# Performance work log

Measured on AMD Instinct MI355X. Metric: run time of the kernel, lower is better.

Reference implementation:

```python
import jax, jax.numpy as jnp
import numpy as np


def _reduce1(x):
    # x: [B, n, d] -> [B, 2d]; exists=max, forall=min over objects (exclude_self is a no-op for cnt=1)
    return jnp.concatenate([x.max(axis=1), x.min(axis=1)], axis=-1)


def _reduce2(x):
    # x: [B, n, n, d] -> [B, n, 2d]; exclude_self masks diagonal i==j (0 for exists/max, 1 for forall/min)
    n = x.shape[1]
    diag = jnp.eye(n, dtype=bool)[None, :, :, None]
    exists = jnp.where(diag, 0.0, x).max(axis=2)
    forall = jnp.where(diag, 1.0, x).min(axis=2)
    return jnp.concatenate([exists, forall], axis=-1)


def _layer(f0, f1, f2, p):
    # One LogicLayer step (breadth=2, minmax reducer, exclude_self, sigmoid norm, no hidden layers)
    W0, b0, W1, b1, W2, b2 = p
    B, n, d1 = f1.shape
    # order 0: [self, reduce(order1)]
    g0 = jnp.concatenate([f0, _reduce1(f1)], axis=-1)
    o0 = jax.nn.sigmoid(g0 @ W0 + b0)
    # order 1: [expand(order0), self, reduce(order2)]
    e0 = jnp.broadcast_to(f0[:, None, :], (B, n, f0.shape[-1]))
    g1 = jnp.concatenate([e0, f1, _reduce2(f2)], axis=-1)
    o1 = jax.nn.sigmoid(g1 @ W1 + b1)
    # order 2: [expand(order1), self] then Permutation(2) = cat(x, swap(i,j))
    e1 = jnp.broadcast_to(f1[:, :, None, :], (B, n, n, d1))
    g2 = jnp.concatenate([e1, f2], axis=-1)
    g2 = jnp.concatenate([g2, jnp.swapaxes(g2, 1, 2)], axis=-1)
    o2 = jax.nn.sigmoid(g2 @ W2 + b2)
    return o0, o1, o2


def setup_inputs() -> dict:
    key = jax.random.key(0)
    B, n = 4, 256
    d = [32, 64, 64]
    O = 128
    ks = iter(jax.random.split(key, 64))
    inp = {
        "x0": jax.random.uniform(next(ks), (B, d[0]), dtype=jnp.float32),
        "x1": jax.random.uniform(next(ks), (B, n, d[1]), dtype=jnp.float32),
        "x2": jax.random.uniform(next(ks), (B, n, n, d[2]), dtype=jnp.float32),
    }
    fan_ins = [
        (d[0] + 2 * d[1], d[0] + d[1] + 2 * d[2], 2 * (d[1] + d[2])),  # layer 0
        (O + 2 * O, O + O + 2 * O, 2 * (O + O)),                        # layer 1
        (O + 2 * O, O + O + 2 * O, 2 * (O + O)),                        # layer 2
    ]
    for l, fins in enumerate(fan_ins):
        for o, fin in enumerate(fins):
            inp[f"W{o}_{l}"] = jax.random.normal(next(ks), (fin, O), dtype=jnp.float32) / np.sqrt(fin).astype(np.float32)
            inp[f"b{o}_{l}"] = jnp.zeros((O,), dtype=jnp.float32)
    return inp


def reference(x0, x1, x2,
              W0_0, b0_0, W1_0, b1_0, W2_0, b2_0,
              W0_1, b0_1, W1_1, b1_1, W2_1, b2_1,
              W0_2, b0_2, W1_2, b1_2, W2_2, b2_2):
    f = (x0, x1, x2)
    for p in ((W0_0, b0_0, W1_0, b1_0, W2_0, b2_0),
              (W0_1, b0_1, W1_1, b1_1, W2_1, b2_1),
              (W0_2, b0_2, W1_2, b1_2, W2_2, b2_2)):
        f = _layer(*f, p)
    return f
```

## Files before the change

### kernel.cpp

```cpp
#include <hip/hip_runtime.h>
#include <hip/hip_bf16.h>
#include <cstdint>

#define NN 256
#define NB 4
#define OC 128

using bf16x8_t = __attribute__((ext_vector_type(8))) __bf16;
using f32x4_t  = __attribute__((ext_vector_type(4))) float;

typedef const __attribute__((address_space(1))) uint8_t* gptr1_t;
typedef __attribute__((address_space(3))) uint8_t* lptr3_t;

__device__ __forceinline__ void async_load16(const void* g, void* l) {
  __builtin_amdgcn_global_load_lds((gptr1_t)g, (lptr3_t)l, 16, 0, 0);
}

__device__ __forceinline__ float sigf(float x) {
  return 1.0f / (1.0f + __expf(-x));
}

__device__ __forceinline__ uint16_t f2bf_rne(float f) {
  uint32_t u = __float_as_uint(f);
  uint32_t r = (u + 0x7fffu + ((u >> 16) & 1u)) >> 16;
  return (uint16_t)r;
}

__global__ __launch_bounds__(256) void reduce2_l0_kernel(
    const float* __restrict__ x2, float* __restrict__ r2,
    uint16_t* __restrict__ x2bf) {
  const int bid = blockIdx.x;
  const int b = bid >> 8, i = bid & 255;
  const int tid = threadIdx.x;
  const int q = tid & 15, s = tid >> 4;
  const size_t rowbase = ((size_t)(b * NN + i) * NN) * 64 + q * 4;
  float mx0 = 0.f, mx1 = 0.f, mx2 = 0.f, mx3 = 0.f;
  float mn0 = 1.f, mn1 = 1.f, mn2 = 1.f, mn3 = 1.f;
  for (int j = s; j < NN; j += 16) {
    const float4 x = *(const float4*)(x2 + rowbase + (size_t)j * 64);
    uint2 pk;
    pk.x = (uint32_t)f2bf_rne(x.x) | ((uint32_t)f2bf_rne(x.y) << 16);
    pk.y = (uint32_t)f2bf_rne(x.z) | ((uint32_t)f2bf_rne(x.w) << 16);
    *(uint2*)(x2bf + rowbase + (size_t)j * 64) = pk;
    if (j != i) {
      mx0 = fmaxf(mx0, x.x); mx1 = fmaxf(mx1, x.y);
      mx2 = fmaxf(mx2, x.z); mx3 = fmaxf(mx3, x.w);
      mn0 = fminf(mn0, x.x); mn1 = fminf(mn1, x.y);
      mn2 = fminf(mn2, x.z); mn3 = fminf(mn3, x.w);
    }
  }
  __shared__ float4 smx[256], smn[256];
  smx[tid] = make_float4(mx0, mx1, mx2, mx3);
  smn[tid] = make_float4(mn0, mn1, mn2, mn3);
  __syncthreads();
  if (s == 0) {
    for (int ss = 1; ss < 16; ++ss) {
      float4 a = smx[q + ss * 16], c = smn[q + ss * 16];
      mx0 = fmaxf(mx0, a.x); mx1 = fmaxf(mx1, a.y);
      mx2 = fmaxf(mx2, a.z); mx3 = fmaxf(mx3, a.w);
      mn0 = fminf(mn0, c.x); mn1 = fminf(mn1, c.y);
      mn2 = fminf(mn2, c.z); mn3 = fminf(mn3, c.w);
    }
    float* r = r2 + (size_t)(b * NN + i) * 128;
    r[q * 4 + 0] = mx0; r[q * 4 + 1] = mx1; r[q * 4 + 2] = mx2; r[q * 4 + 3] = mx3;
    r[64 + q * 4 + 0] = mn0; r[64 + q * 4 + 1] = mn1;
    r[64 + q * 4 + 2] = mn2; r[64 + q * 4 + 3] = mn3;
  }
}

__device__ __forceinline__ void emit_wt(const float* __restrict__ W2,
                                        uint16_t* __restrict__ Wt, int d1,
                                        int d2, int idx) {
  const int K = 2 * d2;
  const int nn = idx / K, k = idx - nn * K;
  const int row = (k < d2) ? (d1 + k) : (2 * d1 + d2 + (k - d2));
  Wt[idx] = f2bf_rne(W2[row * OC + nn]);
}

__global__ void prep_wt_all(const float* __restrict__ W20,
                            const float* __restrict__ W21,
                            const float* __restrict__ W22,
                            uint16_t* __restrict__ Wt0,
                            uint16_t* __restrict__ Wt1,
                            uint16_t* __restrict__ Wt2) {
  const int g = blockIdx.x * 256 + threadIdx.x;
  if (g < 16384) emit_wt(W20, Wt0, 64, 64, g);
  else if (g < 16384 + 32768) emit_wt(W21, Wt1, 128, 128, g - 16384);
  else emit_wt(W22, Wt2, 128, 128, g - 49152);
}

template <int D0, int D1, int D2, bool HAS_NEXT>
__global__ __launch_bounds__(256) void small_kernel(
    const float* __restrict__ f0in, const float* __restrict__ f1in,
    const float* __restrict__ r2in, const float* __restrict__ W0,
    const float* __restrict__ b0, const float* __restrict__ W1,
    const float* __restrict__ b1, const float* __restrict__ W2,
    const float* __restrict__ b2, float* __restrict__ f0out,
    float* __restrict__ f1out, float* __restrict__ u, float* __restrict__ v,
    float* __restrict__ r2n) {
  constexpr int FIN1 = D0 + D1 + 2 * D2;
  constexpr int FIN0 = D0 + 2 * D1;
  constexpr int ROWS = 4;
  const int blk = blockIdx.x;
  const int bi0 = blk * ROWS;
  const int b = bi0 >> 8;
  const int tid = threadIdx.x;
  const int c = tid & 127, s = tid >> 7;

  __shared__ float g1[ROWS][FIN1];
  __shared__ float part[3][ROWS][2][128];
  __shared__ float g0[FIN0];
  __shared__ float rmx[256], rmn[256];

  for (int r = 0; r < ROWS; ++r) {
    const int bi = bi0 + r;
    for (int k = tid; k < FIN1; k += 256) {
      float x;
      if (k < D0) x = f0in[b * D0 + k];
      else if (k < D0 + D1) x = f1in[(size_t)bi * D1 + (k - D0)];
      else x = r2in[(size_t)bi * (2 * D2) + (k - D0 - D1)];
      g1[r][k] = x;
    }
  }
  __syncthreads();

  float a1[ROWS] = {0.f, 0.f, 0.f, 0.f};
  constexpr int H1 = FIN1 / 2;
#pragma unroll 4
  for (int k = s * H1; k < s * H1 + H1; ++k) {
    const float w = W1[(size_t)k * OC + c];
#pragma unroll
    for (int r = 0; r < ROWS; ++r) a1[r] += g1[r][k] * w;
  }
  float au[ROWS] = {0.f, 0.f, 0.f, 0.f};
  float av[ROWS] = {0.f, 0.f, 0.f, 0.f};
  constexpr int H2 = D1 / 2;
#pragma unroll 4
  for (int k = s * H2; k < s * H2 + H2; ++k) {
    const float wu = W2[(size_t)k * OC + c];
    const float wv = W2[(size_t)(D1 + D2 + k) * OC + c];
#pragma unroll
    for (int r = 0; r < ROWS; ++r) {
      const float x = g1[r][D0 + k];
      au[r] += x * wu;
      av[r] += x * wv;
    }
  }
#pragma unroll
  for (int r = 0; r < ROWS; ++r) {
    part[0][r][s][c] = a1[r];
    part[1][r][s][c] = au[r];
    part[2][r][s][c] = av[r];
  }
  __syncthreads();
  if (s == 0) {
#pragma unroll
    for (int r = 0; r < ROWS; ++r) {
      const size_t bi = bi0 + r;
      f1out[bi * OC + c] = sigf(a1[r] + part[0][r][1][c] + b1[c]);
      u[bi * OC + c] = au[r] + part[1][r][1][c] + b2[c];
      v[bi * OC + c] = av[r] + part[2][r][1][c];
    }
  }
  if (HAS_NEXT) {
#pragma unroll
    for (int r = 0; r < ROWS; ++r)
      r2n[(size_t)(bi0 + r) * 256 + s * 128 + c] = (s == 0) ? 0.f : 1.f;
  }

  if ((blk & 63) == 0) {
    constexpr int S = 256 / D1;
    const int cc = tid & (D1 - 1), ss = tid / D1;
    float mx = -1e30f, mn = 1e30f;
    for (int j = ss; j < NN; j += S) {
      const float x = f1in[((size_t)b * NN + j) * D1 + cc];
      mx = fmaxf(mx, x); mn = fminf(mn, x);
    }
    rmx[tid] = mx; rmn[tid] = mn;
    __syncthreads();
    if (ss == 0) {
      for (int s2 = 1; s2 < S; ++s2) {
        mx = fmaxf(mx, rmx[cc + s2 * D1]);
        mn = fminf(mn, rmn[cc + s2 * D1]);
      }
      g0[D0 + cc] = mx;
      g0[D0 + D1 + cc] = mn;
    }
    if (tid < D0) g0[tid] = f0in[b * D0 + tid];
    __syncthreads();
    if (tid < OC) {
      float acc = b0[tid];
#pragma unroll 8
      for (int k = 0; k < FIN0; ++k) acc += g0[k] * W0[k * OC + tid];
      f0out[b * OC + tid] = sigf(acc);
    }
  }
}

template <int D2, typename OUT_T, bool REDUCE>
__global__ __launch_bounds__(256, 3) void gemm2_kernel(
    const __hip_bfloat16* __restrict__ f2, const uint16_t* __restrict__ Wt,
    const float* __restrict__ u, const float* __restrict__ v,
    OUT_T* __restrict__ out, float* __restrict__ r2n) {
  constexpr int K = 2 * D2;
  constexpr int NCH = K / 64;
  constexpr bool BF16OUT = (sizeof(OUT_T) == 2);
  constexpr int LDSB = BF16OUT ? (128 * 272) : 32768;
  const int bid = blockIdx.x;
  const int jt = bid & 1, i = (bid >> 1) & 255, b = bid >> 9;
  const int j0 = jt * 128;
  const int tid = threadIdx.x;
  const int wv = tid >> 6, lane = tid & 63;
  const int wr = wv >> 1, wc = wv & 1;
  const int l15 = lane & 15, l4 = lane >> 4;

  __shared__ __align__(16) uint8_t lds[LDSB];
  __shared__ unsigned smax[128], smin[128];
  uint8_t* const ldsA = lds;
  uint8_t* const ldsW = lds + 16384;

  const __hip_bfloat16* A1 = f2 + ((size_t)(b * NN + i) * NN + j0) * D2;
  const __hip_bfloat16* A2 = f2 + ((size_t)(b * NN + j0) * NN + i) * D2;

  f32x4_t acc[4][4];
#pragma unroll
  for (int a = 0; a < 4; ++a)
#pragma unroll
    for (int q = 0; q < 4; ++q) acc[a][q] = (f32x4_t){0.f, 0.f, 0.f, 0.f};

  for (int c = 0; c < NCH; ++c) {
    const int kbg = c * 64;
    const bool second = (kbg >= D2);
    const __hip_bfloat16* Ab = second ? A2 : A1;
    const size_t rstride = second ? (size_t)NN * D2 : (size_t)D2;
    const int kbase = second ? (kbg - D2) : kbg;
#pragma unroll
    for (int q = 0; q < 4; ++q) {
      const int id = wv * 4 + q;
      const int mi = id & 7, ks = id >> 3;
      const int row = mi * 16 + l15;
      const int kk = ks * 32 + l4 * 8;
      async_load16(Ab + (size_t)row * rstride + kbase + kk, ldsA + id * 1024);
    }
#pragma unroll
    for (int q = 0; q < 4; ++q) {
      const int id = wv * 4 + q;
      const int ni = id & 7, ks = id >> 3;
      const int nn2 = ni * 16 + l15;
      const int kk = ks * 32 + l4 * 8;
      async_load16(Wt + (size_t)nn2 * K + kbg + kk, ldsW + id * 1024);
    }
    __syncthreads();
#pragma unroll
    for (int ks = 0; ks < 2; ++ks) {
      bf16x8_t Af[4], Bf[4];
#pragma unroll
      for (int a = 0; a < 4; ++a)
        Af[a] = *(const bf16x8_t*)(ldsA + ((ks * 8 + wr * 4 + a) << 10) + (lane << 4));
#pragma unroll
      for (int q = 0; q < 4; ++q)
        Bf[q] = *(const bf16x8_t*)(ldsW + ((ks * 8 + wc * 4 + q) << 10) + (lane << 4));
#pragma unroll
      for (int a = 0; a < 4; ++a)
#pragma unroll
        for (int q = 0; q < 4; ++q)
          acc[a][q] = __builtin_amdgcn_mfma_f32_16x16x32_bf16(Af[a], Bf[q],
                                                              acc[a][q], 0, 0, 0);
    }
    __syncthreads();
  }

  const size_t bi2 = (size_t)(b * NN + i);
  float uval[4];
#pragma unroll
  for (int q = 0; q < 4; ++q) uval[q] = u[bi2 * OC + wc * 64 + q * 16 + l15];
  const size_t obase = (bi2 * NN + j0) * OC;
  const size_t vbase = (size_t)(b * NN + j0) * OC;

  if (BF16OUT) {
    if (REDUCE && tid < 128) { smax[tid] = 0u; smin[tid] = 0x3f800000u; }
    __syncthreads();
    float lmx[4] = {0.f, 0.f, 0.f, 0.f};
    float lmn[4] = {1.f, 1.f, 1.f, 1.f};
#pragma unroll
    for (int a = 0; a < 4; ++a) {
      const int rowb = wr * 64 + a * 16 + l4 * 4;
#pragma unroll
      for (int r = 0; r < 4; ++r) {
        const int j = rowb + r;
        const bool excl = (j0 + j) == i;
#pragma unroll
        for (int q = 0; q < 4; ++q) {
          const int col = wc * 64 + q * 16 + l15;
          const float x = acc[a][q][r] + uval[q] + v[vbase + (size_t)j * OC + col];
          const float sg = sigf(x);
          *(uint16_t*)(lds + j * 272 + col * 2) = f2bf_rne(sg);
          if (REDUCE && !excl) {
            lmx[q] = fmaxf(lmx[q], sg);
            lmn[q] = fminf(lmn[q], sg);
          }
        }
      }
    }
    if (REDUCE) {
#pragma unroll
      for (int q = 0; q < 4; ++q) {
        const int col = wc * 64 + q * 16 + l15;
        atomicMax(&smax[col], __float_as_uint(lmx[q]));
        atomicMin(&smin[col], __float_as_uint(lmn[q]));
      }
    }
    __syncthreads();
    uint16_t* const outp = (uint16_t*)out;
#pragma unroll
    for (int ci = 0; ci < 8; ++ci) {
      const int chunk = ci * 256 + tid;
      const int row = chunk >> 4, off = chunk & 15;
      const uint4 val = *(const uint4*)(lds + row * 272 + off * 16);
      *(uint4*)(outp + obase + (size_t)row * OC + off * 8) = val;
    }
    if (REDUCE && tid < 128) {
      unsigned* const r2u = (unsigned*)r2n;
      atomicMax(&r2u[bi2 * 256 + tid], smax[tid]);
      atomicMin(&r2u[bi2 * 256 + 128 + tid], smin[tid]);
    }
  } else {
    float* const outp = (float*)out;
#pragma unroll
    for (int a = 0; a < 4; ++a) {
      const int rowb = wr * 64 + a * 16 + l4 * 4;
#pragma unroll
      for (int r = 0; r < 4; ++r) {
        const int j = rowb + r;
#pragma unroll
        for (int q = 0; q < 4; ++q) {
          const int col = wc * 64 + q * 16 + l15;
          const float x = acc[a][q][r] + uval[q] + v[vbase + (size_t)j * OC + col];
          outp[obase + (size_t)j * OC + col] = sigf(x);
        }
      }
    }
  }
}

extern "C" void kernel_launch(void* const* d_in, const int* in_sizes, int n_in,
                              void* d_out, int out_size, void* d_ws,
                              size_t ws_size, hipStream_t stream) {
  const float* x0 = (const float*)d_in[0];
  const float* x1 = (const float*)d_in[1];
  const float* x2 = (const float*)d_in[2];
  const float *Wp[3][3], *bp[3][3];
  for (int l = 0; l < 3; ++l)
    for (int o = 0; o < 3; ++o) {
      Wp[l][o] = (const float*)d_in[3 + l * 6 + o * 2];
      bp[l][o] = (const float*)d_in[3 + l * 6 + o * 2 + 1];
    }

  const size_t F2E = (size_t)NB * NN * NN * OC;
  const size_t X2E = (size_t)NB * NN * NN * 64;

  uint8_t* ws = (uint8_t*)d_ws;
  size_t off = 0;
  auto carve = [&](size_t bytes) -> uint8_t* {
    uint8_t* p = ws + off;
    off += (bytes + 255) & ~(size_t)255;
    return p;
  };
  float* f0a = (float*)carve((size_t)NB * OC * 4);
  float* f0b = (float*)carve((size_t)NB * OC * 4);
  float* f1a = (float*)carve((size_t)NB * NN * OC * 4);
  float* f1b = (float*)carve((size_t)NB * NN * OC * 4);
  float* r2a = (float*)carve((size_t)NB * NN * 128 * 4);
  float* r2b = (float*)carve((size_t)NB * NN * 256 * 4);
  float* r2c = (float*)carve((size_t)NB * NN * 256 * 4);
  float* uu  = (float*)carve((size_t)NB * NN * OC * 4);
  float* vv  = (float*)carve((size_t)NB * NN * OC * 4);
  uint16_t* Wt0 = (uint16_t*)carve((size_t)OC * 128 * 2);
  uint16_t* Wt1 = (uint16_t*)carve((size_t)OC * 256 * 2);
  uint16_t* Wt2 = (uint16_t*)carve((size_t)OC * 256 * 2);
  __hip_bfloat16* f2a = (__hip_bfloat16*)carve(F2E * 2);

  __hip_bfloat16* f2b;
  uint16_t* x2bf;
  if (ws_size >= off + F2E * 2) {
    f2b = (__hip_bfloat16*)carve(F2E * 2);
    x2bf = (uint16_t*)f2b;
  } else {
    f2b = (__hip_bfloat16*)d_in[2];
    x2bf = (uint16_t*)carve(X2E * 2);
  }

  float* out_f0 = (float*)d_out;
  float* out_f1 = out_f0 + (size_t)NB * OC;
  float* out_f2 = out_f1 + (size_t)NB * NN * OC;

  prep_wt_all<<<320, 256, 0, stream>>>(Wp[0][2], Wp[1][2], Wp[2][2], Wt0, Wt1,
                                       Wt2);
  reduce2_l0_kernel<<<NB * NN, 256, 0, stream>>>(x2, r2a, x2bf);

  small_kernel<32, 64, 64, true><<<NB * NN / 4, 256, 0, stream>>>(
      x0, x1, r2a, Wp[0][0], bp[0][0], Wp[0][1], bp[0][1], Wp[0][2], bp[0][2],
      f0a, f1a, uu, vv, r2b);
  gemm2_kernel<64, __hip_bfloat16, true><<<NB * NN * 2, 256, 0, stream>>>(
      (const __hip_bfloat16*)x2bf, Wt0, uu, vv, f2a, r2b);

  small_kernel<128, 128, 128, true><<<NB * NN / 4, 256, 0, stream>>>(
      f0a, f1a, r2b, Wp[1][0], bp[1][0], Wp[1][1], bp[1][1], Wp[1][2], bp[1][2],
      f0b, f1b, uu, vv, r2c);
  gemm2_kernel<128, __hip_bfloat16, true><<<NB * NN * 2, 256, 0, stream>>>(
      f2a, Wt1, uu, vv, f2b, r2c);

  small_kernel<128, 128, 128, false><<<NB * NN / 4, 256, 0, stream>>>(
      f0b, f1b, r2c, Wp[2][0], bp[2][0], Wp[2][1], bp[2][1], Wp[2][2], bp[2][2],
      out_f0, out_f1, uu, vv, nullptr);
  gemm2_kernel<128, float, false><<<NB * NN * 2, 256, 0, stream>>>(
      f2b, Wt2, uu, vv, out_f2, nullptr);
}
```

Before: 584.8 us.

## Replace scalar order-0/1 small kernel with bf16 MFMA GEMM on packed inputs

Replaces the per-layer scalar FP32 small_kernel, which computed the order-1 linear layer and the u/v projections, with a bf16 MFMA GEMM. Its operands are a packed bf16 activation matrix and a bf16 weight matrix built once at startup from W1 and W2. Order-0 work moves to a separate tiny kernel that also broadcasts f0 into the next layer's packed input. A small conversion kernel packs the reduced r2 into the same buffer. The aim is to cut the FP32 FMA cost of the small matmuls, at the price of bf16 rounding on order-1 inputs, several extra launches, and only 48 blocks in the GEMM.

```diff
diff --git a/kernel.cpp b/kernel.cpp
--- a/kernel.cpp
+++ b/kernel.cpp
@@ -26,14 +26,62 @@
   return (uint16_t)r;
 }
 
+__device__ __forceinline__ void emit_wt(const float* __restrict__ W2,
+                                        uint16_t* __restrict__ Wt, int d1,
+                                        int d2, int idx) {
+  const int K = 2 * d2;
+  const int nn = idx / K, k = idx - nn * K;
+  const int row = (k < d2) ? (d1 + k) : (2 * d1 + d2 + (k - d2));
+  Wt[idx] = f2bf_rne(W2[row * OC + nn]);
+}
+
+__device__ __forceinline__ void emit_bt(const float* __restrict__ W1,
+                                        const float* __restrict__ W2,
+                                        uint16_t* __restrict__ Bt, int D0,
+                                        int D1, int D2, int FIN1, int KP,
+                                        int idx) {
+  const int n = idx / KP, k = idx - n * KP;
+  float val = 0.f;
+  if (n < 128) {
+    if (k < FIN1) val = W1[k * OC + n];
+  } else if (n < 256) {
+    if (k >= D0 && k < D0 + D1) val = W2[(k - D0) * OC + (n - 128)];
+  } else {
+    if (k >= D0 && k < D0 + D1) val = W2[(D1 + D2 + (k - D0)) * OC + (n - 256)];
+  }
+  Bt[idx] = f2bf_rne(val);
+}
+
+__global__ __launch_bounds__(256) void prep_all(
+    const float* __restrict__ W2_0, const float* __restrict__ W2_1,
+    const float* __restrict__ W2_2, const float* __restrict__ W1_0,
+    const float* __restrict__ W1_1, const float* __restrict__ W1_2,
+    uint16_t* __restrict__ Wt0, uint16_t* __restrict__ Wt1,
+    uint16_t* __restrict__ Wt2, uint16_t* __restrict__ Bt0,
+    uint16_t* __restrict__ Bt1, uint16_t* __restrict__ Bt2) {
+  int g = blockIdx.x * 256 + threadIdx.x;
+  if (g < 16384) { emit_wt(W2_0, Wt0, 64, 64, g); return; }
+  g -= 16384;
+  if (g < 32768) { emit_wt(W2_1, Wt1, 128, 128, g); return; }
+  g -= 32768;
+  if (g < 32768) { emit_wt(W2_2, Wt2, 128, 128, g); return; }
+  g -= 32768;
+  if (g < 98304) { emit_bt(W1_0, W2_0, Bt0, 32, 64, 64, 224, 256, g); return; }
+  g -= 98304;
+  if (g < 196608) { emit_bt(W1_1, W2_1, Bt1, 128, 128, 128, 512, 512, g); return; }
+  g -= 196608;
+  if (g < 196608) { emit_bt(W1_2, W2_2, Bt2, 128, 128, 128, 512, 512, g); }
+}
+
 __global__ __launch_bounds__(256) void reduce2_l0_kernel(
-    const float* __restrict__ x2, float* __restrict__ r2,
-    uint16_t* __restrict__ x2bf) {
+    const float* __restrict__ x2, const float* __restrict__ x0,
+    const float* __restrict__ x1, uint16_t* __restrict__ g1bf0,
+    uint16_t* __restrict__ x2bf, float* __restrict__ r2init) {
   const int bid = blockIdx.x;
   const int b = bid >> 8, i = bid & 255;
   const int tid = threadIdx.x;
   const int q = tid & 15, s = tid >> 4;
-  const size_t rowbase = ((size_t)(b * NN + i) * NN) * 64 + q * 4;
+  const size_t rowbase = ((size_t)bid * NN) * 64 + q * 4;
   float mx0 = 0.f, mx1 = 0.f, mx2 = 0.f, mx3 = 0.f;
   float mn0 = 1.f, mn1 = 1.f, mn2 = 1.f, mn3 = 1.f;
   for (int j = s; j < NN; j += 16) {
@@ -53,6 +101,7 @@
   smx[tid] = make_float4(mx0, mx1, mx2, mx3);
   smn[tid] = make_float4(mn0, mn1, mn2, mn3);
   __syncthreads();
+  uint16_t* const g = g1bf0 + (size_t)bid * 256;
   if (s == 0) {
     for (int ss = 1; ss < 16; ++ss) {
       float4 a = smx[q + ss * 16], c = smn[q + ss * 16];
@@ -61,140 +110,161 @@
       mn0 = fminf(mn0, c.x); mn1 = fminf(mn1, c.y);
       mn2 = fminf(mn2, c.z); mn3 = fminf(mn3, c.w);
     }
-    float* r = r2 + (size_t)(b * NN + i) * 128;
-    r[q * 4 + 0] = mx0; r[q * 4 + 1] = mx1; r[q * 4 + 2] = mx2; r[q * 4 + 3] = mx3;
-    r[64 + q * 4 + 0] = mn0; r[64 + q * 4 + 1] = mn1;
-    r[64 + q * 4 + 2] = mn2; r[64 + q * 4 + 3] = mn3;
-  }
-}
-
-__device__ __forceinline__ void emit_wt(const float* __restrict__ W2,
-                                        uint16_t* __restrict__ Wt, int d1,
-                                        int d2, int idx) {
-  const int K = 2 * d2;
-  const int nn = idx / K, k = idx - nn * K;
-  const int row = (k < d2) ? (d1 + k) : (2 * d1 + d2 + (k - d2));
-  Wt[idx] = f2bf_rne(W2[row * OC + nn]);
-}
-
-__global__ void prep_wt_all(const float* __restrict__ W20,
-                            const float* __restrict__ W21,
-                            const float* __restrict__ W22,
-                            uint16_t* __restrict__ Wt0,
-                            uint16_t* __restrict__ Wt1,
-                            uint16_t* __restrict__ Wt2) {
-  const int g = blockIdx.x * 256 + threadIdx.x;
-  if (g < 16384) emit_wt(W20, Wt0, 64, 64, g);
-  else if (g < 16384 + 32768) emit_wt(W21, Wt1, 128, 128, g - 16384);
-  else emit_wt(W22, Wt2, 128, 128, g - 49152);
-}
-
-template <int D0, int D1, int D2, bool HAS_NEXT>
-__global__ __launch_bounds__(256) void small_kernel(
-    const float* __restrict__ f0in, const float* __restrict__ f1in,
-    const float* __restrict__ r2in, const float* __restrict__ W0,
-    const float* __restrict__ b0, const float* __restrict__ W1,
-    const float* __restrict__ b1, const float* __restrict__ W2,
-    const float* __restrict__ b2, float* __restrict__ f0out,
-    float* __restrict__ f1out, float* __restrict__ u, float* __restrict__ v,
-    float* __restrict__ r2n) {
-  constexpr int FIN1 = D0 + D1 + 2 * D2;
-  constexpr int FIN0 = D0 + 2 * D1;
-  constexpr int ROWS = 4;
-  const int blk = blockIdx.x;
-  const int bi0 = blk * ROWS;
-  const int b = bi0 >> 8;
+    g[96 + q * 4 + 0] = f2bf_rne(mx0); g[96 + q * 4 + 1] = f2bf_rne(mx1);
+    g[96 + q * 4 + 2] = f2bf_rne(mx2); g[96 + q * 4 + 3] = f2bf_rne(mx3);
+    g[160 + q * 4 + 0] = f2bf_rne(mn0); g[160 + q * 4 + 1] = f2bf_rne(mn1);
+    g[160 + q * 4 + 2] = f2bf_rne(mn2); g[160 + q * 4 + 3] = f2bf_rne(mn3);
+  }
+  if (tid < 32) g[tid] = f2bf_rne(x0[b * 32 + tid]);
+  else if (tid < 96) g[tid] = f2bf_rne(x1[(size_t)bid * 64 + tid - 32]);
+  else if (tid >= 224) g[tid] = 0;
+  r2init[(size_t)bid * 256 + tid] = (tid < 128) ? 0.f : 1.f;
+}
+
+template <int D0, int D1, bool DUP>
+__global__ __launch_bounds__(256) void o0_kernel(
+    const float* __restrict__ f0, const float* __restrict__ f1,
+    const float* __restrict__ W0, const float* __restrict__ b0,
+    float* __restrict__ f0out, uint16_t* __restrict__ g1next) {
+  constexpr int FIN = D0 + 2 * D1;
+  constexpr int S = 256 / D1;
+  const int b = blockIdx.x;
   const int tid = threadIdx.x;
-  const int c = tid & 127, s = tid >> 7;
-
-  __shared__ float g1[ROWS][FIN1];
-  __shared__ float part[3][ROWS][2][128];
-  __shared__ float g0[FIN0];
-  __shared__ float rmx[256], rmn[256];
-
-  for (int r = 0; r < ROWS; ++r) {
-    const int bi = bi0 + r;
-    for (int k = tid; k < FIN1; k += 256) {
-      float x;
-      if (k < D0) x = f0in[b * D0 + k];
-      else if (k < D0 + D1) x = f1in[(size_t)bi * D1 + (k - D0)];
-      else x = r2in[(size_t)bi * (2 * D2) + (k - D0 - D1)];
-      g1[r][k] = x;
-    }
-  }
-  __syncthreads();
-
-  float a1[ROWS] = {0.f, 0.f, 0.f, 0.f};
-  constexpr int H1 = FIN1 / 2;
-#pragma unroll 4
-  for (int k = s * H1; k < s * H1 + H1; ++k) {
-    const float w = W1[(size_t)k * OC + c];
-#pragma unroll
-    for (int r = 0; r < ROWS; ++r) a1[r] += g1[r][k] * w;
-  }
-  float au[ROWS] = {0.f, 0.f, 0.f, 0.f};
-  float av[ROWS] = {0.f, 0.f, 0.f, 0.f};
-  constexpr int H2 = D1 / 2;
-#pragma unroll 4
-  for (int k = s * H2; k < s * H2 + H2; ++k) {
-    const float wu = W2[(size_t)k * OC + c];
-    const float wv = W2[(size_t)(D1 + D2 + k) * OC + c];
-#pragma unroll
-    for (int r = 0; r < ROWS; ++r) {
-      const float x = g1[r][D0 + k];
-      au[r] += x * wu;
-      av[r] += x * wv;
-    }
-  }
-#pragma unroll
-  for (int r = 0; r < ROWS; ++r) {
-    part[0][r][s][c] = a1[r];
-    part[1][r][s][c] = au[r];
-    part[2][r][s][c] = av[r];
-  }
+  const int c = tid & (D1 - 1), s = tid / D1;
+  __shared__ float g0[FIN];
+  __shared__ float smx[256], smn[256];
+  __shared__ float sval[128];
+  float mx = -1e30f, mn = 1e30f;
+  const float* f1b = f1 + (size_t)b * NN * D1;
+  for (int j = s; j < NN; j += S) {
+    float x = f1b[(size_t)j * D1 + c];
+    mx = fmaxf(mx, x); mn = fminf(mn, x);
+  }
+  smx[tid] = mx; smn[tid] = mn;
   __syncthreads();
   if (s == 0) {
-#pragma unroll
-    for (int r = 0; r < ROWS; ++r) {
-      const size_t bi = bi0 + r;
-      f1out[bi * OC + c] = sigf(a1[r] + part[0][r][1][c] + b1[c]);
-      u[bi * OC + c] = au[r] + part[1][r][1][c] + b2[c];
-      v[bi * OC + c] = av[r] + part[2][r][1][c];
-    }
-  }
-  if (HAS_NEXT) {
-#pragma unroll
-    for (int r = 0; r < ROWS; ++r)
-      r2n[(size_t)(bi0 + r) * 256 + s * 128 + c] = (s == 0) ? 0.f : 1.f;
-  }
-
-  if ((blk & 63) == 0) {
-    constexpr int S = 256 / D1;
-    const int cc = tid & (D1 - 1), ss = tid / D1;
-    float mx = -1e30f, mn = 1e30f;
-    for (int j = ss; j < NN; j += S) {
-      const float x = f1in[((size_t)b * NN + j) * D1 + cc];
-      mx = fmaxf(mx, x); mn = fminf(mn, x);
-    }
-    rmx[tid] = mx; rmn[tid] = mn;
-    __syncthreads();
-    if (ss == 0) {
-      for (int s2 = 1; s2 < S; ++s2) {
-        mx = fmaxf(mx, rmx[cc + s2 * D1]);
-        mn = fminf(mn, rmn[cc + s2 * D1]);
+    for (int ss = 1; ss < S; ++ss) {
+      mx = fmaxf(mx, smx[c + ss * D1]);
+      mn = fminf(mn, smn[c + ss * D1]);
+    }
+    g0[D0 + c] = mx;
+    g0[D0 + D1 + c] = mn;
+  }
+  if (tid < D0) g0[tid] = f0[b * D0 + tid];
+  __syncthreads();
+  if (tid < OC) {
+    float acc = b0[tid];
+#pragma unroll 8
+    for (int k = 0; k < FIN; ++k) acc += g0[k] * W0[k * OC + tid];
+    const float val = sigf(acc);
+    f0out[b * OC + tid] = val;
+    sval[tid] = val;
+  }
+  if (DUP) {
+    __syncthreads();
+    for (int idx = tid; idx < 256 * 128; idx += 256) {
+      const int row = idx >> 7, cc = idx & 127;
+      g1next[((size_t)(b * 256 + row)) * 512 + cc] = f2bf_rne(sval[cc]);
+    }
+  }
+}
+
+template <int KP, bool DUP>
+__global__ __launch_bounds__(256) void small_gemm(
+    const uint16_t* __restrict__ g1, const uint16_t* __restrict__ Bt,
+    const float* __restrict__ b1, const float* __restrict__ b2,
+    float* __restrict__ f1out, uint16_t* __restrict__ g1next,
+    float* __restrict__ u, float* __restrict__ v) {
+  constexpr int NCH = KP / 64;
+  const int bid = blockIdx.x;
+  const int mt = bid / 3, nt = bid - mt * 3;
+  const int m0 = mt * 64, n0 = nt * 128;
+  const int tid = threadIdx.x;
+  const int wv = tid >> 6, lane = tid & 63;
+  const int l15 = lane & 15, l4 = lane >> 4;
+
+  __shared__ __align__(16) uint8_t ldsA[8192];
+  __shared__ __align__(16) uint8_t ldsB[16384];
+
+  f32x4_t acc[4][2];
+#pragma unroll
+  for (int a = 0; a < 4; ++a)
+#pragma unroll
+    for (int q = 0; q < 2; ++q) acc[a][q] = (f32x4_t){0.f, 0.f, 0.f, 0.f};
+
+  for (int c = 0; c < NCH; ++c) {
+    const int kbg = c * 64;
+#pragma unroll
+    for (int t = 0; t < 2; ++t) {
+      const int id = wv * 2 + t;
+      const int mi = id & 3, ks = id >> 2;
+      async_load16(g1 + (size_t)(m0 + mi * 16 + l15) * KP + kbg + ks * 32 + l4 * 8,
+                   ldsA + id * 1024);
+    }
+#pragma unroll
+    for (int t = 0; t < 4; ++t) {
+      const int id = wv * 4 + t;
+      const int ni = id & 7, ks = id >> 3;
+      async_load16(Bt + (size_t)(n0 + ni * 16 + l15) * KP + kbg + ks * 32 + l4 * 8,
+                   ldsB + id * 1024);
+    }
+    __syncthreads();
+#pragma unroll
+    for (int ks = 0; ks < 2; ++ks) {
+      bf16x8_t Af[4], Bf[2];
+#pragma unroll
+      for (int a = 0; a < 4; ++a)
+        Af[a] = *(const bf16x8_t*)(ldsA + ((ks * 4 + a) << 10) + (lane << 4));
+#pragma unroll
+      for (int q = 0; q < 2; ++q)
+        Bf[q] = *(const bf16x8_t*)(ldsB + ((ks * 8 + wv * 2 + q) << 10) + (lane << 4));
+#pragma unroll
+      for (int a = 0; a < 4; ++a)
+#pragma unroll
+        for (int q = 0; q < 2; ++q)
+          acc[a][q] = __builtin_amdgcn_mfma_f32_16x16x32_bf16(Af[a], Bf[q],
+                                                              acc[a][q], 0, 0, 0);
+    }
+    __syncthreads();
+  }
+
+  float bias[2];
+#pragma unroll
+  for (int q = 0; q < 2; ++q) {
+    const int cc = wv * 32 + q * 16 + l15;
+    bias[q] = (nt == 0) ? b1[cc] : ((nt == 1) ? b2[cc] : 0.f);
+  }
+#pragma unroll
+  for (int a = 0; a < 4; ++a) {
+    const int rl = a * 16 + l4 * 4;
+#pragma unroll
+    for (int r = 0; r < 4; ++r) {
+      const size_t bi = m0 + rl + r;
+#pragma unroll
+      for (int q = 0; q < 2; ++q) {
+        const int cc = wv * 32 + q * 16 + l15;
+        const float x = acc[a][q][r] + bias[q];
+        if (nt == 0) {
+          const float val = sigf(x);
+          f1out[bi * OC + cc] = val;
+          if (DUP) g1next[bi * 512 + 128 + cc] = f2bf_rne(val);
+        } else if (nt == 1) {
+          u[bi * OC + cc] = x;
+        } else {
+          v[bi * OC + cc] = x;
+        }
       }
-      g0[D0 + cc] = mx;
-      g0[D0 + D1 + cc] = mn;
-    }
-    if (tid < D0) g0[tid] = f0in[b * D0 + tid];
-    __syncthreads();
-    if (tid < OC) {
-      float acc = b0[tid];
-#pragma unroll 8
-      for (int k = 0; k < FIN0; ++k) acc += g0[k] * W0[k * OC + tid];
-      f0out[b * OC + tid] = sigf(acc);
-    }
-  }
+    }
+  }
+}
+
+template <bool INIT_NEXT>
+__global__ __launch_bounds__(256) void conv_r2_kernel(
+    const float* __restrict__ r2, uint16_t* __restrict__ g1next,
+    float* __restrict__ r2next) {
+  const int bi = blockIdx.x, t = threadIdx.x;
+  g1next[(size_t)bi * 512 + 256 + t] = f2bf_rne(r2[(size_t)bi * 256 + t]);
+  if (INIT_NEXT) r2next[(size_t)bi * 256 + t] = (t < 128) ? 0.f : 1.f;
 }
 
 template <int D2, typename OUT_T, bool REDUCE>
@@ -370,7 +440,6 @@
   float* f0b = (float*)carve((size_t)NB * OC * 4);
   float* f1a = (float*)carve((size_t)NB * NN * OC * 4);
   float* f1b = (float*)carve((size_t)NB * NN * OC * 4);
-  float* r2a = (float*)carve((size_t)NB * NN * 128 * 4);
   float* r2b = (float*)carve((size_t)NB * NN * 256 * 4);
   float* r2c = (float*)carve((size_t)NB * NN * 256 * 4);
   float* uu  = (float*)carve((size_t)NB * NN * OC * 4);
@@ -378,6 +447,12 @@
   uint16_t* Wt0 = (uint16_t*)carve((size_t)OC * 128 * 2);
   uint16_t* Wt1 = (uint16_t*)carve((size_t)OC * 256 * 2);
   uint16_t* Wt2 = (uint16_t*)carve((size_t)OC * 256 * 2);
+  uint16_t* Bt0 = (uint16_t*)carve((size_t)384 * 256 * 2);
+  uint16_t* Bt1 = (uint16_t*)carve((size_t)384 * 512 * 2);
+  uint16_t* Bt2 = (uint16_t*)carve((size_t)384 * 512 * 2);
+  uint16_t* g1bf0 = (uint16_t*)carve((size_t)NB * NN * 256 * 2);
+  uint16_t* g1bf1 = (uint16_t*)carve((size_t)NB * NN * 512 * 2);
+  uint16_t* g1bf2 = (uint16_t*)carve((size_t)NB * NN * 512 * 2);
   __hip_bfloat16* f2a = (__hip_bfloat16*)carve(F2E * 2);
 
   __hip_bfloat16* f2b;
@@ -394,25 +469,31 @@
   float* out_f1 = out_f0 + (size_t)NB * OC;
   float* out_f2 = out_f1 + (size_t)NB * NN * OC;
 
-  prep_wt_all<<<320, 256, 0, stream>>>(Wp[0][2], Wp[1][2], Wp[2][2], Wt0, Wt1,
-                                       Wt2);
-  reduce2_l0_kernel<<<NB * NN, 256, 0, stream>>>(x2, r2a, x2bf);
-
-  small_kernel<32, 64, 64, true><<<NB * NN / 4, 256, 0, stream>>>(
-      x0, x1, r2a, Wp[0][0], bp[0][0], Wp[0][1], bp[0][1], Wp[0][2], bp[0][2],
-      f0a, f1a, uu, vv, r2b);
+  prep_all<<<2240, 256, 0, stream>>>(Wp[0][2], Wp[1][2], Wp[2][2], Wp[0][1],
+                                     Wp[1][1], Wp[2][1], Wt0, Wt1, Wt2, Bt0,
+                                     Bt1, Bt2);
+  reduce2_l0_kernel<<<NB * NN, 256, 0, stream>>>(x2, x0, x1, g1bf0, x2bf, r2b);
+
+  o0_kernel<32, 64, true><<<NB, 256, 0, stream>>>(x0, x1, Wp[0][0], bp[0][0],
+                                                  f0a, g1bf1);
+  small_gemm<256, true><<<48, 256, 0, stream>>>(g1bf0, Bt0, bp[0][1], bp[0][2],
+                                                f1a, g1bf1, uu, vv);
   gemm2_kernel<64, __hip_bfloat16, true><<<NB * NN * 2, 256, 0, stream>>>(
       (const __hip_bfloat16*)x2bf, Wt0, uu, vv, f2a, r2b);
-
-  small_kernel<128, 128, 128, true><<<NB * NN / 4, 256, 0, stream>>>(
-      f0a, f1a, r2b, Wp[1][0], bp[1][0], Wp[1][1], bp[1][1], Wp[1][2], bp[1][2],
-      f0b, f1b, uu, vv, r2c);
+  conv_r2_kernel<true><<<NB * NN, 256, 0, stream>>>(r2b, g1bf1, r2c);
+
+  o0_kernel<128, 128, true><<<NB, 256, 0, stream>>>(f0a, f1a, Wp[1][0],
+                                                    bp[1][0], f0b, g1bf2);
+  small_gemm<512, true><<<48, 256, 0, stream>>>(g1bf1, Bt1, bp[1][1], bp[1][2],
+                                                f1b, g1bf2, uu, vv);
   gemm2_kernel<128, __hip_bfloat16, true><<<NB * NN * 2, 256, 0, stream>>>(
       f2a, Wt1, uu, vv, f2b, r2c);
-
-  small_kernel<128, 128, 128, false><<<NB * NN / 4, 256, 0, stream>>>(
-      f0b, f1b, r2c, Wp[2][0], bp[2][0], Wp[2][1], bp[2][1], Wp[2][2], bp[2][2],
-      out_f0, out_f1, uu, vv, nullptr);
+  conv_r2_kernel<false><<<NB * NN, 256, 0, stream>>>(r2c, g1bf2, nullptr);
+
+  o0_kernel<128, 128, false><<<NB, 256, 0, stream>>>(f0b, f1b, Wp[2][0],
+                                                     bp[2][0], out_f0, nullptr);
+  small_gemm<512, false><<<48, 256, 0, stream>>>(g1bf2, Bt2, bp[2][1], bp[2][2],
+                                                 out_f1, nullptr, uu, vv);
   gemm2_kernel<128, float, false><<<NB * NN * 2, 256, 0, stream>>>(
       f2b, Wt2, uu, vv, out_f2, nullptr);
 }
```

Result: faster. 539.7 us (-7.7%).
